# Optimization experiments

Measured on AMD Instinct MI355X. Metric: run time of the kernel, lower is better.

The kernel has to match this reference:

```python
import jax, jax.numpy as jnp
import numpy as np

N, B, D, K_IN, P = 64, 256, 1792, 35, 10
EPS = 1e-5


def setup_inputs() -> dict:
    key = jax.random.key(0)
    ks = jax.random.split(key, 8)
    s_tok = 1.0 / np.sqrt(K_IN)
    s_net = 1.0 / np.sqrt(D)
    return {
        "X": jax.random.normal(ks[0], (N, B, D), dtype=jnp.float32),
        "task_id": jax.random.normal(ks[1], (B, K_IN), dtype=jnp.float32),
        # tokens: Linear(35, 10*1792)
        "W_tok": jax.random.uniform(ks[2], (P * D, K_IN), jnp.float32, -s_tok, s_tok),
        "b_tok": jax.random.uniform(ks[3], (P * D,), jnp.float32, -s_tok, s_tok),
        # ptokens: Linear(35, 1792)
        "W_ptok": jax.random.uniform(ks[4], (D, K_IN), jnp.float32, -s_tok, s_tok),
        "b_ptok": jax.random.uniform(ks[5], (D,), jnp.float32, -s_tok, s_tok),
        # LayerNorm(1792)
        "gamma": jnp.ones((D,), jnp.float32),
        "beta": jnp.zeros((D,), jnp.float32),
        # net: Linear(1792, 10)
        "W_net": jax.random.uniform(ks[6], (P, D), jnp.float32, -s_net, s_net),
        "b_net": jax.random.uniform(ks[7], (P,), jnp.float32, -s_net, s_net),
    }


def _layernorm(x, gamma, beta):
    mu = jnp.mean(x, axis=-1, keepdims=True)
    var = jnp.mean(jnp.square(x - mu), axis=-1, keepdims=True)
    return (x - mu) * jax.lax.rsqrt(var + EPS) * gamma + beta


def reference(X, task_id, W_tok, b_tok, W_ptok, b_ptok, gamma, beta, W_net, b_net):
    # ptokens(task_id): (b, D); identical across n, so compute once and broadcast.
    ptok = task_id @ W_ptok.T + b_ptok                       # (b, D)
    task_token = _layernorm(ptok[None, :, :] + X, gamma, beta)  # (n, b, D)
    # net -> sigmoid: per-token mixing weights over P prompts.
    weight = jax.nn.sigmoid(task_token @ W_net.T + b_net)    # (n, b, P)
    # tokens(task_id): (b, P, D); identical across n, broadcast in einsum.
    prompt_bank = (task_id @ W_tok.T + b_tok).reshape(B, P, D)  # (b, P, D)
    prompt = jnp.einsum("nbp,bpd->nbd", weight, prompt_bank)  # (n, b, D)
    return X + prompt
```

## Files before the change

### kernel.cpp

```cpp
#include <hip/hip_runtime.h>
#include <hip/hip_bf16.h>

#define NN 64
#define BB 256
#define DD 1792
#define KK 35
#define PP 10
#define DQ 448
#define GR 4
#define NGRP 28

__device__ __forceinline__ float group16_sum_dpp(float x) {
    asm("v_add_f32_dpp %0, %0, %0 row_shr:1 row_mask:0xf bank_mask:0xf bound_ctrl:0" : "+v"(x));
    asm("v_add_f32_dpp %0, %0, %0 row_shr:2 row_mask:0xf bank_mask:0xf bound_ctrl:0" : "+v"(x));
    asm("v_add_f32_dpp %0, %0, %0 row_shr:4 row_mask:0xf bank_mask:0xf bound_ctrl:0" : "+v"(x));
    asm("v_add_f32_dpp %0, %0, %0 row_shr:8 row_mask:0xf bank_mask:0xf bound_ctrl:0" : "+v"(x));
    return x;
}

#define PIN4(v) asm volatile("" : "+v"(v.x), "+v"(v.y), "+v"(v.z), "+v"(v.w))
#define PIN1(s) asm volatile("" : "+v"(s))

__global__ void prep_gf(const float* __restrict__ gamma, const float* __restrict__ beta,
                        const float* __restrict__ Wnet, const float* __restrict__ bnet,
                        float* __restrict__ GF, float* __restrict__ SG, float* __restrict__ ZC) {
    const int p = blockIdx.x;
    const int tid = threadIdx.x;
    float sg = 0.f, sb = 0.f;
#pragma unroll
    for (int j = 0; j < 7; ++j) {
        int d = j * 256 + tid;
        float wv = Wnet[p * DD + d];
        float g = gamma[d] * wv;
        GF[p * DD + d] = g;
        sg += g;
        sb += beta[d] * wv;
    }
#pragma unroll
    for (int off = 32; off > 0; off >>= 1) {
        sg += __shfl_xor(sg, off);
        sb += __shfl_xor(sb, off);
    }
    __shared__ float rs[4][2];
    if ((tid & 63) == 0) { rs[tid >> 6][0] = sg; rs[tid >> 6][1] = sb; }
    __syncthreads();
    if (tid == 0) {
        float a = 0.f, c = 0.f;
#pragma unroll
        for (int w = 0; w < 4; ++w) { a += rs[w][0]; c += rs[w][1]; }
        SG[p] = a;
        ZC[p] = c + bnet[p];
    }
}

__global__ void prep_bank(const float* __restrict__ task,
                          const float* __restrict__ Wtok, const float* __restrict__ btok,
                          const float* __restrict__ Wptok, const float* __restrict__ bptok,
                          float* __restrict__ bank, float* __restrict__ ptok) {
    __shared__ float ti[32 * KK];
    const int tid = threadIdx.x;
    const int b0 = blockIdx.y * 32;
    for (int i = tid; i < 32 * KK; i += 256) ti[i] = task[b0 * KK + i];

    const int r = blockIdx.x * 256 + tid;
    const bool isbank = (r < PP * DD);
    const int rr = isbank ? r : (r - PP * DD);
    const float* __restrict__ W = isbank ? Wtok : Wptok;
    const float bias = isbank ? btok[r] : bptok[rr];

    float w[KK];
#pragma unroll
    for (int k = 0; k < KK; ++k) w[k] = W[rr * KK + k];

    __syncthreads();
#pragma unroll 1
    for (int bb = 0; bb < 32; ++bb) {
        float acc = bias;
#pragma unroll
        for (int k = 0; k < KK; ++k) acc = fmaf(ti[bb * KK + k], w[k], acc);
        const int b = b0 + bb;
        if (isbank) bank[b * (PP * DD) + r] = acc;
        else        ptok[b * DD + rr]       = acc;
    }
}

__global__ __launch_bounds__(448) void fused_lds(
    const float* __restrict__ X, const float* __restrict__ BANK,
    const float* __restrict__ PTOK, const float* __restrict__ GF,
    const float* __restrict__ SG, const float* __restrict__ ZC,
    float* __restrict__ OUT) {
    const int tid  = threadIdx.x;
    const int lane = tid & 63;
    const int c    = tid >> 6;
    const int b    = blockIdx.x & (BB - 1);
    const int half = blockIdx.x >> 8;
    const int n0   = half * 32;

    const float4* __restrict__ X4 = (const float4*)X;
    const float4* __restrict__ B4 = (const float4*)BANK;
    const float4* __restrict__ G4 = (const float4*)GF;
    const float4* __restrict__ P4 = (const float4*)PTOK;
    float4* __restrict__ O4 = (float4*)OUT;

    __shared__ float xbuf[2][GR][DD];
    __shared__ float red[GR][NGRP][12];
    __shared__ float wlds[GR][PP];

    const size_t rstride = (size_t)BB * DQ;
    const size_t gbase = (size_t)b * DQ + c * 64 + lane;

#define STAGE(BUF, GN)                                                             \
    {                                                                              \
        _Pragma("unroll")                                                          \
        for (int r = 0; r < GR; ++r) {                                             \
            const float4* src = X4 + (size_t)(n0 + (GN) * GR + r) * rstride + gbase;\
            __builtin_amdgcn_global_load_lds(                                      \
                (const __attribute__((address_space(1))) void*)src,                \
                (__attribute__((address_space(3))) void*)&xbuf[BUF][r][c * 256],   \
                16, 0, 0);                                                         \
        }                                                                          \
        __builtin_amdgcn_sched_barrier(0);                                         \
    }

    STAGE(0, 0)

    float4 ptk = P4[gbase];
    float4 gf[PP];
#pragma unroll
    for (int p = 0; p < PP; ++p) gf[p] = G4[(size_t)p * DQ + c * 64 + lane];
    float4 bk[PP];
#pragma unroll
    for (int p = 0; p < PP; ++p) bk[p] = B4[((size_t)b * PP + p) * DQ + c * 64 + lane];
    const int vv = tid & 15;
    float sgv = 0.f, zcv = 0.f;
    if (tid < GR * 16 && vv >= 2 && vv < 12) { sgv = SG[vv - 2]; zcv = ZC[vv - 2]; }

    PIN4(ptk);
#pragma unroll
    for (int p = 0; p < PP; ++p) { PIN4(gf[p]); PIN4(bk[p]); }
    PIN1(sgv); PIN1(zcv);

    const bool writer = ((lane & 15) == 15);
    const int g16 = tid >> 4;

#pragma unroll 1
    for (int g = 0; g < 8; ++g) {
        if (g < 7) STAGE((g + 1) & 1, g + 1)

        if (g < 7) { asm volatile("s_waitcnt vmcnt(8)" ::: "memory"); }
        else       { asm volatile("s_waitcnt vmcnt(4)" ::: "memory"); }
        __builtin_amdgcn_sched_barrier(0);

        const int cur = g & 1;

#pragma unroll
        for (int r = 0; r < GR; ++r) {
            const float4 x = *(const float4*)&xbuf[cur][r][c * 256 + lane * 4];
            float4 t;
            t.x = x.x + ptk.x; t.y = x.y + ptk.y;
            t.z = x.z + ptk.z; t.w = x.w + ptk.w;

            float s1 = t.x + t.y + t.z + t.w;
            float s2 = t.x * t.x;
            s2 = fmaf(t.y, t.y, s2); s2 = fmaf(t.z, t.z, s2); s2 = fmaf(t.w, t.w, s2);
            float a[PP];
#pragma unroll
            for (int p = 0; p < PP; ++p) {
                float v = t.x * gf[p].x;
                v = fmaf(t.y, gf[p].y, v);
                v = fmaf(t.z, gf[p].z, v);
                v = fmaf(t.w, gf[p].w, v);
                a[p] = v;
            }
            s1 = group16_sum_dpp(s1);
            s2 = group16_sum_dpp(s2);
#pragma unroll
            for (int p = 0; p < PP; ++p) a[p] = group16_sum_dpp(a[p]);

            if (writer) {
                float4* dst = (float4*)&red[r][g16][0];
                dst[0] = make_float4(s1, s2, a[0], a[1]);
                dst[1] = make_float4(a[2], a[3], a[4], a[5]);
                dst[2] = make_float4(a[6], a[7], a[8], a[9]);
            }
        }

        asm volatile("s_waitcnt lgkmcnt(0)" ::: "memory");
        __builtin_amdgcn_sched_barrier(0);
        __builtin_amdgcn_s_barrier();
        __builtin_amdgcn_sched_barrier(0);

        if (tid < GR * 16) {
            const int row = tid >> 4;
            float f = 0.f;
            if (vv < 12) {
#pragma unroll
                for (int q = 0; q < NGRP; ++q) f += red[row][q][vv];
            }
            const int bse = (tid & 63) & ~15;
            const float mu = __shfl(f, bse)     * (1.0f / (float)DD);
            const float ms = __shfl(f, bse + 1) * (1.0f / (float)DD);
            const float istd = rsqrtf(ms - mu * mu + 1e-5f);
            if (vv >= 2 && vv < 12) {
                const float z = istd * (f - mu * sgv) + zcv;
                wlds[row][vv - 2] = 1.0f / (1.0f + __expf(-z));
            }
        }

        asm volatile("s_waitcnt lgkmcnt(0)" ::: "memory");
        __builtin_amdgcn_sched_barrier(0);
        __builtin_amdgcn_s_barrier();
        __builtin_amdgcn_sched_barrier(0);

#pragma unroll
        for (int r = 0; r < GR; ++r) {
            const float4 x = *(const float4*)&xbuf[cur][r][c * 256 + lane * 4];
            float4 acc = x;
#pragma unroll
            for (int p = 0; p < PP; ++p) {
                const float wv = wlds[r][p];
                acc.x = fmaf(wv, bk[p].x, acc.x);
                acc.y = fmaf(wv, bk[p].y, acc.y);
                acc.z = fmaf(wv, bk[p].z, acc.z);
                acc.w = fmaf(wv, bk[p].w, acc.w);
            }
            O4[(size_t)(n0 + g * GR + r) * rstride + gbase] = acc;
        }
    }
#undef STAGE
}

extern "C" void kernel_launch(void* const* d_in, const int* in_sizes, int n_in,
                              void* d_out, int out_size, void* d_ws, size_t ws_size,
                              hipStream_t stream) {
    const float* X     = (const float*)d_in[0];
    const float* task  = (const float*)d_in[1];
    const float* Wtok  = (const float*)d_in[2];
    const float* btok  = (const float*)d_in[3];
    const float* Wptok = (const float*)d_in[4];
    const float* bptok = (const float*)d_in[5];
    const float* gamma = (const float*)d_in[6];
    const float* beta  = (const float*)d_in[7];
    const float* Wnet  = (const float*)d_in[8];
    const float* bnet  = (const float*)d_in[9];
    float* out = (float*)d_out;

    float* ws = (float*)d_ws;
    float* bank = ws;
    float* ptok = bank + (size_t)BB * PP * DD;
    float* GF   = ptok + (size_t)BB * DD;
    float* SG   = GF + PP * DD;
    float* ZC   = SG + PP;

    prep_gf<<<PP, 256, 0, stream>>>(gamma, beta, Wnet, bnet, GF, SG, ZC);
    prep_bank<<<dim3(77, 8), 256, 0, stream>>>(task, Wtok, btok, Wptok, bptok, bank, ptok);
    fused_lds<<<2 * BB, 448, 0, stream>>>(X, bank, ptok, GF, SG, ZC, out);
}
```

Measured before the change: 90.99 us.

## Merge two n-halves into one 896-thread block and use nontemporal output stores

The fused kernel now launches one 896-thread block per batch element, with two 448-thread teams each handling half of the n range. Team-indexed LDS buffers and shared barriers replace the previous two separate blocks. Output writes become nontemporal stores to reduce cache pollution, and the register-pinning asm is removed. Because the teams share block-wide barriers they run in lockstep, and each block now needs twice the LDS, which may limit occupancy.

```diff
diff --git a/kernel.cpp b/kernel.cpp
--- a/kernel.cpp
+++ b/kernel.cpp
@@ -9,6 +9,9 @@
 #define DQ 448
 #define GR 4
 #define NGRP 28
+#define NTH 896
+
+typedef float fx4 __attribute__((ext_vector_type(4)));
 
 __device__ __forceinline__ float group16_sum_dpp(float x) {
     asm("v_add_f32_dpp %0, %0, %0 row_shr:1 row_mask:0xf bank_mask:0xf bound_ctrl:0" : "+v"(x));
@@ -17,9 +20,6 @@
     asm("v_add_f32_dpp %0, %0, %0 row_shr:8 row_mask:0xf bank_mask:0xf bound_ctrl:0" : "+v"(x));
     return x;
 }
-
-#define PIN4(v) asm volatile("" : "+v"(v.x), "+v"(v.y), "+v"(v.z), "+v"(v.w))
-#define PIN1(s) asm volatile("" : "+v"(s))
 
 __global__ void prep_gf(const float* __restrict__ gamma, const float* __restrict__ beta,
                         const float* __restrict__ Wnet, const float* __restrict__ bnet,
@@ -84,27 +84,29 @@
     }
 }
 
-__global__ __launch_bounds__(448) void fused_lds(
+__global__ __launch_bounds__(NTH, 1) __attribute__((amdgpu_waves_per_eu(4)))
+void fused_lds2(
     const float* __restrict__ X, const float* __restrict__ BANK,
     const float* __restrict__ PTOK, const float* __restrict__ GF,
     const float* __restrict__ SG, const float* __restrict__ ZC,
     float* __restrict__ OUT) {
     const int tid  = threadIdx.x;
-    const int lane = tid & 63;
-    const int c    = tid >> 6;
-    const int b    = blockIdx.x & (BB - 1);
-    const int half = blockIdx.x >> 8;
-    const int n0   = half * 32;
+    const int team = (tid >= 448) ? 1 : 0;
+    const int ttid = tid - team * 448;
+    const int lane = ttid & 63;
+    const int c    = ttid >> 6;
+    const int b    = blockIdx.x;
+    const int nbase = team * 32;
 
     const float4* __restrict__ X4 = (const float4*)X;
     const float4* __restrict__ B4 = (const float4*)BANK;
     const float4* __restrict__ G4 = (const float4*)GF;
     const float4* __restrict__ P4 = (const float4*)PTOK;
-    float4* __restrict__ O4 = (float4*)OUT;
-
-    __shared__ float xbuf[2][GR][DD];
-    __shared__ float red[GR][NGRP][12];
-    __shared__ float wlds[GR][PP];
+    fx4* __restrict__ OO = (fx4*)OUT;
+
+    __shared__ float xbuf[2][2][GR][DD];
+    __shared__ float red[2][GR][NGRP][12];
+    __shared__ float wlds[2][GR][PP];
 
     const size_t rstride = (size_t)BB * DQ;
     const size_t gbase = (size_t)b * DQ + c * 64 + lane;
@@ -113,10 +115,10 @@
     {                                                                              \
         _Pragma("unroll")                                                          \
         for (int r = 0; r < GR; ++r) {                                             \
-            const float4* src = X4 + (size_t)(n0 + (GN) * GR + r) * rstride + gbase;\
+            const float4* src = X4 + (size_t)(nbase + (GN) * GR + r) * rstride + gbase; \
             __builtin_amdgcn_global_load_lds(                                      \
                 (const __attribute__((address_space(1))) void*)src,                \
-                (__attribute__((address_space(3))) void*)&xbuf[BUF][r][c * 256],   \
+                (__attribute__((address_space(3))) void*)&xbuf[team][BUF][r][c * 256], \
                 16, 0, 0);                                                         \
         }                                                                          \
         __builtin_amdgcn_sched_barrier(0);                                         \
@@ -124,24 +126,19 @@
 
     STAGE(0, 0)
 
-    float4 ptk = P4[gbase];
+    const float4 ptk = P4[gbase];
     float4 gf[PP];
 #pragma unroll
     for (int p = 0; p < PP; ++p) gf[p] = G4[(size_t)p * DQ + c * 64 + lane];
     float4 bk[PP];
 #pragma unroll
     for (int p = 0; p < PP; ++p) bk[p] = B4[((size_t)b * PP + p) * DQ + c * 64 + lane];
-    const int vv = tid & 15;
+    const int vv = ttid & 15;
     float sgv = 0.f, zcv = 0.f;
-    if (tid < GR * 16 && vv >= 2 && vv < 12) { sgv = SG[vv - 2]; zcv = ZC[vv - 2]; }
-
-    PIN4(ptk);
-#pragma unroll
-    for (int p = 0; p < PP; ++p) { PIN4(gf[p]); PIN4(bk[p]); }
-    PIN1(sgv); PIN1(zcv);
+    if (ttid < GR * 16 && vv >= 2 && vv < 12) { sgv = SG[vv - 2]; zcv = ZC[vv - 2]; }
 
     const bool writer = ((lane & 15) == 15);
-    const int g16 = tid >> 4;
+    const int g16 = ttid >> 4;
 
 #pragma unroll 1
     for (int g = 0; g < 8; ++g) {
@@ -155,7 +152,7 @@
 
 #pragma unroll
         for (int r = 0; r < GR; ++r) {
-            const float4 x = *(const float4*)&xbuf[cur][r][c * 256 + lane * 4];
+            const float4 x = *(const float4*)&xbuf[team][cur][r][c * 256 + lane * 4];
             float4 t;
             t.x = x.x + ptk.x; t.y = x.y + ptk.y;
             t.z = x.z + ptk.z; t.w = x.w + ptk.w;
@@ -178,7 +175,7 @@
             for (int p = 0; p < PP; ++p) a[p] = group16_sum_dpp(a[p]);
 
             if (writer) {
-                float4* dst = (float4*)&red[r][g16][0];
+                float4* dst = (float4*)&red[team][r][g16][0];
                 dst[0] = make_float4(s1, s2, a[0], a[1]);
                 dst[1] = make_float4(a[2], a[3], a[4], a[5]);
                 dst[2] = make_float4(a[6], a[7], a[8], a[9]);
@@ -190,20 +187,20 @@
         __builtin_amdgcn_s_barrier();
         __builtin_amdgcn_sched_barrier(0);
 
-        if (tid < GR * 16) {
-            const int row = tid >> 4;
+        if (ttid < GR * 16) {
+            const int row = ttid >> 4;
             float f = 0.f;
             if (vv < 12) {
 #pragma unroll
-                for (int q = 0; q < NGRP; ++q) f += red[row][q][vv];
-            }
-            const int bse = (tid & 63) & ~15;
+                for (int q = 0; q < NGRP; ++q) f += red[team][row][q][vv];
+            }
+            const int bse = (ttid & 63) & ~15;
             const float mu = __shfl(f, bse)     * (1.0f / (float)DD);
             const float ms = __shfl(f, bse + 1) * (1.0f / (float)DD);
             const float istd = rsqrtf(ms - mu * mu + 1e-5f);
             if (vv >= 2 && vv < 12) {
                 const float z = istd * (f - mu * sgv) + zcv;
-                wlds[row][vv - 2] = 1.0f / (1.0f + __expf(-z));
+                wlds[team][row][vv - 2] = 1.0f / (1.0f + __expf(-z));
             }
         }
 
@@ -214,17 +211,19 @@
 
 #pragma unroll
         for (int r = 0; r < GR; ++r) {
-            const float4 x = *(const float4*)&xbuf[cur][r][c * 256 + lane * 4];
+            const float4 x = *(const float4*)&xbuf[team][cur][r][c * 256 + lane * 4];
             float4 acc = x;
 #pragma unroll
             for (int p = 0; p < PP; ++p) {
-                const float wv = wlds[r][p];
+                const float wv = wlds[team][r][p];
                 acc.x = fmaf(wv, bk[p].x, acc.x);
                 acc.y = fmaf(wv, bk[p].y, acc.y);
                 acc.z = fmaf(wv, bk[p].z, acc.z);
                 acc.w = fmaf(wv, bk[p].w, acc.w);
             }
-            O4[(size_t)(n0 + g * GR + r) * rstride + gbase] = acc;
+            fx4 av; av.x = acc.x; av.y = acc.y; av.z = acc.z; av.w = acc.w;
+            __builtin_nontemporal_store(av,
+                &OO[(size_t)(nbase + g * GR + r) * rstride + gbase]);
         }
     }
 #undef STAGE
@@ -254,5 +253,5 @@
 
     prep_gf<<<PP, 256, 0, stream>>>(gamma, beta, Wnet, bnet, GF, SG, ZC);
     prep_bank<<<dim3(77, 8), 256, 0, stream>>>(task, Wtok, btok, Wptok, bptok, bank, ptok);
-    fused_lds<<<2 * BB, 448, 0, stream>>>(X, bank, ptok, GF, SG, ZC, out);
-}
+    fused_lds2<<<BB, NTH, 0, stream>>>(X, bank, ptok, GF, SG, ZC, out);
+}
```

Result: faster. 78.32 us (-13.9%).
